# Performance work log

Hardware: AMD Instinct MI355X
Metric: run time of the kernel (lower is better)

Reference implementation:

```python
import jax, jax.numpy as jnp
import numpy as np

B, N, OBS, ACT, RET, E, OUT, K = 128, 1_000_000, 64, 16, 8, 64, 64, 16
MEM = OBS + ACT + RET  # 88


def setup_inputs() -> dict:
    key = jax.random.key(0)
    k0, k1, k2, k3 = jax.random.split(key, 4)
    obs = jax.random.normal(k0, (B, OBS), dtype=jnp.float32)
    memories = jax.random.normal(k1, (N, MEM), dtype=jnp.float32)
    W_obs = jax.random.normal(k2, (OBS, E), dtype=jnp.float32) * 0.05
    b_obs = jnp.zeros((E,), dtype=jnp.float32)
    W_out = jax.random.normal(k3, (E + ACT, OUT), dtype=jnp.float32) * 0.05
    b_out = jnp.zeros((OUT,), dtype=jnp.float32)
    return {"obs": obs, "memories": memories, "W_obs": W_obs, "b_obs": b_obs,
            "W_out": W_out, "b_out": b_out}


def reference(obs, memories, W_obs, b_obs, W_out, b_out):
    obs_len = W_obs.shape[0]          # 64
    embed_dim = W_obs.shape[1]        # 64
    act_len = W_out.shape[0] - embed_dim  # 16
    k = K

    obs_mem = memories[:, :obs_len]                              # [N, OBS]
    # f.normalize: L2-normalize each memory's observation part (eps as in torch)
    norm = jnp.maximum(jnp.linalg.norm(obs_mem, axis=-1, keepdims=True), 1e-12)
    m = obs_mem / norm                                           # [N, OBS], unit rows
    # squared L2 distance via expansion: |o|^2 + |m|^2 - 2 o.m  (|m|^2 == 1)
    # sqrt is monotonic, so top-k on squared distances gives identical indices.
    sq = (jnp.sum(obs * obs, axis=-1, keepdims=True) + 1.0
          - 2.0 * obs @ m.T)                                     # [B, N]
    _, idx = jax.lax.top_k(-sq, k)                               # k nearest, [B, k]

    sim_mems = memories[idx]                                     # [B, k, MEM]
    sim_act = sim_mems[..., obs_len:obs_len + act_len]           # [B, k, ACT]
    sim_ret = sim_mems[..., obs_len + act_len:]                  # [B, k, RET]
    ret_sum = jnp.sum(sim_ret, axis=-1)                          # [B, k]
    best = jnp.argmax(ret_sum, axis=-1)                          # [B]
    best_acts = jnp.take_along_axis(sim_act, best[:, None, None], axis=1)[:, 0]  # [B, ACT]

    obs_embeded = jnp.tanh(obs @ W_obs + b_obs)                  # [B, E]
    embed_best = jnp.concatenate([obs_embeded, best_acts], axis=-1)  # [B, E+ACT]
    logits = jnp.tanh(embed_best @ W_out + b_out)                # [B, OUT]
    return logits
```

## Files before the change

kernel.cpp:

```cpp
#include <hip/hip_runtime.h>
#include <cstdint>

#define B_    128
#define N_    1000000
#define OBS_  64
#define MEM_  88
#define ACT_  16
#define RET_  8
#define E_    64
#define OUT_  64
#define K_    16
#define CAP_  6144
#define P_    32
#define PCAP_ 256
#define CHUNKS_ (N_ / 16)
#define NBLK_  768
#define NWAVE_ (NBLK_ * 4)

typedef float    f32x4 __attribute__((ext_vector_type(4)));
typedef _Float16 f16x8 __attribute__((ext_vector_type(8)));
typedef uint32_t u32x4v __attribute__((ext_vector_type(4)));

__device__ __forceinline__ f16x8 pack8(float4 a, float4 b) {
    u32x4v u;
    u.x = __builtin_bit_cast(uint32_t, __builtin_amdgcn_cvt_pkrtz(a.x, a.y));
    u.y = __builtin_bit_cast(uint32_t, __builtin_amdgcn_cvt_pkrtz(a.z, a.w));
    u.z = __builtin_bit_cast(uint32_t, __builtin_amdgcn_cvt_pkrtz(b.x, b.y));
    u.w = __builtin_bit_cast(uint32_t, __builtin_amdgcn_cvt_pkrtz(b.z, b.w));
    return __builtin_bit_cast(f16x8, u);
}

__global__ __launch_bounds__(256, 3) void filter_kernel(const float* __restrict__ obs,
                                                        const float* __restrict__ memories,
                                                        int* __restrict__ cnt2,
                                                        int* __restrict__ cand2) {
    __shared__ float sThr[B_];

    const int tid  = threadIdx.x;
    const int lane = tid & 63;
    const int wv   = tid >> 6;
    const int fr   = lane & 15;
    const int fc   = lane >> 4;

    if (tid < B_) {
        const float4* orow = reinterpret_cast<const float4*>(obs + tid * OBS_);
        float s = 0.f;
        #pragma unroll
        for (int i = 0; i < 16; ++i) {
            float4 q = orow[i];
            s += q.x * q.x + q.y * q.y + q.z * q.z + q.w * q.w;
        }
        sThr[tid] = 0.45f * sqrtf(s);
    }

    f16x8 A0[8], A1[8];
    #pragma unroll
    for (int blk = 0; blk < 8; ++blk) {
        const float* p = obs + (blk * 16 + fr) * OBS_ + fc * 8;
        float4 q0 = *(const float4*)(p);
        float4 q1 = *(const float4*)(p + 4);
        float4 q2 = *(const float4*)(p + 32);
        float4 q3 = *(const float4*)(p + 36);
        A0[blk] = pack8(q0, q1);
        A1[blk] = pack8(q2, q3);
    }
    __syncthreads();

    float tmin[8];
    #pragma unroll
    for (int blk = 0; blk < 8; ++blk) {
        const float4 t = *reinterpret_cast<const float4*>(&sThr[blk * 16 + fc * 4]);
        tmin[blk] = fminf(fminf(t.x, t.y), fminf(t.z, t.w));
    }

    const int wid  = blockIdx.x * 4 + wv;
    const int part = wid & (P_ - 1);
    int* __restrict__ pcnt  = cnt2 + part * B_;
    int* __restrict__ pcand = cand2 + part * B_ * PCAP_;

    const int start = (int)((long long)wid * CHUNKS_ / NWAVE_);
    const int end   = (int)((long long)(wid + 1) * CHUNKS_ / NWAVE_);

    const int loff = fc * 8;

    float4 c0, c1, c2, c3, d0, d1, d2, d3;
    {
        const float* m = memories + (size_t)(start * 16 + fr) * MEM_ + loff;
        c0 = *(const float4*)(m);      c1 = *(const float4*)(m + 4);
        c2 = *(const float4*)(m + 32); c3 = *(const float4*)(m + 36);
    }
    {
        const float* m = memories + (size_t)((start + 1) * 16 + fr) * MEM_ + loff;
        d0 = *(const float4*)(m);      d1 = *(const float4*)(m + 4);
        d2 = *(const float4*)(m + 32); d3 = *(const float4*)(m + 36);
    }
    float nm;
    {
        float nq = c0.x*c0.x + c0.y*c0.y + c0.z*c0.z + c0.w*c0.w
                 + c1.x*c1.x + c1.y*c1.y + c1.z*c1.z + c1.w*c1.w
                 + c2.x*c2.x + c2.y*c2.y + c2.z*c2.z + c2.w*c2.w
                 + c3.x*c3.x + c3.y*c3.y + c3.z*c3.z + c3.w*c3.w;
        nq += __shfl_xor(nq, 16, 64);
        nq += __shfl_xor(nq, 32, 64);
        nm = sqrtf(nq);
    }

    for (int chunk = start; chunk < end; ++chunk) {
        int nc = chunk + 2;
        nc = (nc < end) ? nc : chunk;
        float4 e0, e1, e2, e3;
        {
            const float* m = memories + (size_t)(nc * 16 + fr) * MEM_ + loff;
            e0 = *(const float4*)(m);      e1 = *(const float4*)(m + 4);
            e2 = *(const float4*)(m + 32); e3 = *(const float4*)(m + 36);
        }

        float nqd = d0.x*d0.x + d0.y*d0.y + d0.z*d0.z + d0.w*d0.w
                  + d1.x*d1.x + d1.y*d1.y + d1.z*d1.z + d1.w*d1.w
                  + d2.x*d2.x + d2.y*d2.y + d2.z*d2.z + d2.w*d2.w
                  + d3.x*d3.x + d3.y*d3.y + d3.z*d3.z + d3.w*d3.w;
        nqd += __shfl_xor(nqd, 16, 64);
        nqd += __shfl_xor(nqd, 32, 64);

        const int gm = chunk * 16 + fr;
        const f16x8 b0 = pack8(c0, c1);
        const f16x8 b1 = pack8(c2, c3);

        #pragma unroll
        for (int blk = 0; blk < 8; ++blk) {
            f32x4 acc = {0.f, 0.f, 0.f, 0.f};
            acc = __builtin_amdgcn_mfma_f32_16x16x32_f16(A0[blk], b0, acc, 0, 0, 0);
            acc = __builtin_amdgcn_mfma_f32_16x16x32_f16(A1[blk], b1, acc, 0, 0, 0);
            const float m4 = fmaxf(fmaxf(acc[0], acc[1]), fmaxf(acc[2], acc[3]));
            if (m4 >= tmin[blk] * nm) {
                const float4 t = *reinterpret_cast<const float4*>(&sThr[blk * 16 + fc * 4]);
                const int rb = blk * 16 + fc * 4;
                if (acc[0] >= t.x * nm) { int p = atomicAdd(&pcnt[rb + 0], 1); if (p < PCAP_) pcand[(rb + 0) * PCAP_ + p] = gm; }
                if (acc[1] >= t.y * nm) { int p = atomicAdd(&pcnt[rb + 1], 1); if (p < PCAP_) pcand[(rb + 1) * PCAP_ + p] = gm; }
                if (acc[2] >= t.z * nm) { int p = atomicAdd(&pcnt[rb + 2], 1); if (p < PCAP_) pcand[(rb + 2) * PCAP_ + p] = gm; }
                if (acc[3] >= t.w * nm) { int p = atomicAdd(&pcnt[rb + 3], 1); if (p < PCAP_) pcand[(rb + 3) * PCAP_ + p] = gm; }
            }
        }

        c0 = d0; c1 = d1; c2 = d2; c3 = d3;
        d0 = e0; d1 = e1; d2 = e2; d3 = e3;
        nm = sqrtf(nqd);
    }
}

__global__ __launch_bounds__(256) void refine_kernel(const float* __restrict__ obs,
                                                     const float* __restrict__ memories,
                                                     const float* __restrict__ W_obs,
                                                     const float* __restrict__ b_obs,
                                                     const float* __restrict__ W_out,
                                                     const float* __restrict__ b_out,
                                                     const int* __restrict__ cnt2,
                                                     const int* __restrict__ cand2,
                                                     float* __restrict__ out) {
    __shared__ __align__(16) float sObs[OBS_];
    __shared__ unsigned long long sKey[CAP_];
    __shared__ int   pCnt[P_];
    __shared__ int   pBase[P_];
    __shared__ int   sN;
    __shared__ int   selIdx[K_];
    __shared__ float sRet[K_];
    __shared__ float sEmb[E_ + ACT_];
    __shared__ int   sBest;

    const int b   = blockIdx.x;
    const int tid = threadIdx.x;

    if (tid < OBS_) sObs[tid] = obs[b * OBS_ + tid];
    if (tid < P_) {
        int c = cnt2[tid * B_ + b];
        pCnt[tid] = (c > PCAP_) ? PCAP_ : c;
    }
    __syncthreads();
    if (tid == 0) {
        int off = 0;
        for (int p = 0; p < P_; ++p) { pBase[p] = off; off += pCnt[p]; }
        sN = (off > CAP_) ? CAP_ : off;
    }
    __syncthreads();
    const int n = sN;

    for (int p = 0; p < P_; ++p) {
        const int c = pCnt[p], base = pBase[p];
        for (int i = tid; i < c; i += 256) {
            int dst = base + i;
            if (dst < CAP_) sKey[dst] = (unsigned long long)(unsigned)cand2[(p * B_ + b) * PCAP_ + i];
        }
    }
    __syncthreads();

    for (int i = tid; i < n; i += 256) {
        int idx = (int)(unsigned)sKey[i];
        const float* mrow = memories + (size_t)idx * MEM_;
        float dot = 0.f, nq = 0.f;
        #pragma unroll
        for (int c = 0; c < OBS_; c += 4) {
            float4 mv = *reinterpret_cast<const float4*>(mrow + c);
            float4 ov = *reinterpret_cast<const float4*>(&sObs[c]);
            dot += mv.x * ov.x + mv.y * ov.y + mv.z * ov.z + mv.w * ov.w;
            nq  += mv.x * mv.x + mv.y * mv.y + mv.z * mv.z + mv.w * mv.w;
        }
        float sc = dot / fmaxf(sqrtf(nq), 1e-12f);
        uint32_t sb = __float_as_uint(sc);
        sb ^= (sb & 0x80000000u) ? 0xFFFFFFFFu : 0x80000000u;
        sKey[i] = ((unsigned long long)sb << 32) | (unsigned long long)(0xFFFFFFFFu - (uint32_t)idx);
    }
    __syncthreads();

    if (tid < 64) {
        for (int k = 0; k < K_; ++k) {
            unsigned long long best = 0ull; int bpos = -1;
            for (int i = tid; i < n; i += 64) {
                unsigned long long v = sKey[i];
                if (v > best) { best = v; bpos = i; }
            }
            #pragma unroll
            for (int off = 32; off > 0; off >>= 1) {
                unsigned long long ov = __shfl_xor(best, off, 64);
                int op = __shfl_xor(bpos, off, 64);
                if (ov > best) { best = ov; bpos = op; }
            }
            if (tid == 0) {
                selIdx[k] = (bpos >= 0) ? (int)(0xFFFFFFFFu - (uint32_t)(best & 0xFFFFFFFFull)) : -1;
                if (bpos >= 0) sKey[bpos] = 0ull;
            }
            __builtin_amdgcn_wave_barrier();
        }
    }
    __syncthreads();

    if (tid < K_) {
        int ix = selIdx[tid];
        float rs = -1e30f;
        if (ix >= 0) {
            rs = 0.f;
            #pragma unroll
            for (int j = 0; j < RET_; ++j)
                rs += memories[(size_t)ix * MEM_ + OBS_ + ACT_ + j];
        }
        sRet[tid] = rs;
    }
    __syncthreads();
    if (tid == 0) {
        float best = sRet[0]; int bk = 0;
        for (int k = 1; k < K_; ++k)
            if (sRet[k] > best) { best = sRet[k]; bk = k; }
        int bix = selIdx[bk];
        sBest = (bix >= 0) ? bix : 0;
    }
    __syncthreads();

    if (tid < E_) {
        float a = b_obs[tid];
        for (int c = 0; c < OBS_; ++c) a += sObs[c] * W_obs[c * E_ + tid];
        sEmb[tid] = tanhf(a);
    } else if (tid < E_ + ACT_) {
        int j = tid - E_;
        sEmb[tid] = memories[(size_t)sBest * MEM_ + OBS_ + j];
    }
    __syncthreads();

    if (tid < OUT_) {
        float a = b_out[tid];
        for (int c = 0; c < E_ + ACT_; ++c) a += sEmb[c] * W_out[c * OUT_ + tid];
        out[b * OUT_ + tid] = tanhf(a);
    }
}

extern "C" void kernel_launch(void* const* d_in, const int* in_sizes, int n_in,
                              void* d_out, int out_size, void* d_ws, size_t ws_size,
                              hipStream_t stream) {
    const float* obs      = (const float*)d_in[0];
    const float* memories = (const float*)d_in[1];
    const float* W_obs    = (const float*)d_in[2];
    const float* b_obs    = (const float*)d_in[3];
    const float* W_out    = (const float*)d_in[4];
    const float* b_out    = (const float*)d_in[5];
    float* out = (float*)d_out;

    char* ws    = (char*)d_ws;
    int*   cnt2 = (int*)ws;
    int*   cand2 = (int*)(ws + P_ * B_ * 4);

    hipMemsetAsync(cnt2, 0, P_ * B_ * sizeof(int), stream);
    filter_kernel<<<NBLK_, 256, 0, stream>>>(obs, memories, cnt2, cand2);
    refine_kernel<<<B_, 256, 0, stream>>>(obs, memories, W_obs, b_obs, W_out, b_out,
                                          cnt2, cand2, out);
}
```

Measured before the change: 111.6 us.

## Stage 32-row memory chunks through per-wave LDS with coalesced loads

```diff
diff --git a/kernel.cpp b/kernel.cpp
--- a/kernel.cpp
+++ b/kernel.cpp
@@ -13,13 +13,18 @@
 #define CAP_  6144
 #define P_    32
 #define PCAP_ 256
-#define CHUNKS_ (N_ / 16)
+#define ROWS_PC_ 32
+#define CHUNKS32_ (N_ / ROWS_PC_)
 #define NBLK_  768
 #define NWAVE_ (NBLK_ * 4)
+#define LDSROW_ 92
+#define LDSCHUNK_ (ROWS_PC_ * LDSROW_)
 
 typedef float    f32x4 __attribute__((ext_vector_type(4)));
 typedef _Float16 f16x8 __attribute__((ext_vector_type(8)));
 typedef uint32_t u32x4v __attribute__((ext_vector_type(4)));
+
+typedef struct { uint4 v[11]; } chunkregs;
 
 __device__ __forceinline__ f16x8 pack8(float4 a, float4 b) {
     u32x4v u;
@@ -35,6 +40,7 @@
                                                         int* __restrict__ cnt2,
                                                         int* __restrict__ cand2) {
     __shared__ float sThr[B_];
+    __shared__ __align__(16) float sMem[4 * LDSCHUNK_];
 
     const int tid  = threadIdx.x;
     const int lane = tid & 63;
@@ -78,73 +84,77 @@
     int* __restrict__ pcnt  = cnt2 + part * B_;
     int* __restrict__ pcand = cand2 + part * B_ * PCAP_;
 
-    const int start = (int)((long long)wid * CHUNKS_ / NWAVE_);
-    const int end   = (int)((long long)(wid + 1) * CHUNKS_ / NWAVE_);
-
-    const int loff = fc * 8;
-
-    float4 c0, c1, c2, c3, d0, d1, d2, d3;
+    const int start = (int)((long long)wid * CHUNKS32_ / NWAVE_);
+    const int end   = (int)((long long)(wid + 1) * CHUNKS32_ / NWAVE_);
+
+    float* __restrict__ lds = sMem + wv * LDSCHUNK_;
+    const uint4* __restrict__ mem4 = reinterpret_cast<const uint4*>(memories);
+
+    chunkregs G;
+
     {
-        const float* m = memories + (size_t)(start * 16 + fr) * MEM_ + loff;
-        c0 = *(const float4*)(m);      c1 = *(const float4*)(m + 4);
-        c2 = *(const float4*)(m + 32); c3 = *(const float4*)(m + 36);
-    }
-    {
-        const float* m = memories + (size_t)((start + 1) * 16 + fr) * MEM_ + loff;
-        d0 = *(const float4*)(m);      d1 = *(const float4*)(m + 4);
-        d2 = *(const float4*)(m + 32); d3 = *(const float4*)(m + 36);
-    }
-    float nm;
-    {
-        float nq = c0.x*c0.x + c0.y*c0.y + c0.z*c0.z + c0.w*c0.w
-                 + c1.x*c1.x + c1.y*c1.y + c1.z*c1.z + c1.w*c1.w
-                 + c2.x*c2.x + c2.y*c2.y + c2.z*c2.z + c2.w*c2.w
-                 + c3.x*c3.x + c3.y*c3.y + c3.z*c3.z + c3.w*c3.w;
-        nq += __shfl_xor(nq, 16, 64);
-        nq += __shfl_xor(nq, 32, 64);
-        nm = sqrtf(nq);
-    }
-
-    for (int chunk = start; chunk < end; ++chunk) {
-        int nc = chunk + 2;
-        nc = (nc < end) ? nc : chunk;
-        float4 e0, e1, e2, e3;
+        const uint4* src = mem4 + (size_t)start * 704;
+        #pragma unroll
+        for (int i = 0; i < 11; ++i) G.v[i] = src[i * 64 + lane];
+        #pragma unroll
+        for (int i = 0; i < 11; ++i) {
+            int j = i * 64 + lane;
+            int row = j / 22, slot = j - row * 22;
+            *reinterpret_cast<uint4*>(&lds[row * LDSROW_ + slot * 4]) = G.v[i];
+        }
+    }
+
+    for (int t = start; t < end; ++t) {
+        const int nt = (t + 1 < end) ? (t + 1) : t;
         {
-            const float* m = memories + (size_t)(nc * 16 + fr) * MEM_ + loff;
-            e0 = *(const float4*)(m);      e1 = *(const float4*)(m + 4);
-            e2 = *(const float4*)(m + 32); e3 = *(const float4*)(m + 36);
-        }
-
-        float nqd = d0.x*d0.x + d0.y*d0.y + d0.z*d0.z + d0.w*d0.w
-                  + d1.x*d1.x + d1.y*d1.y + d1.z*d1.z + d1.w*d1.w
-                  + d2.x*d2.x + d2.y*d2.y + d2.z*d2.z + d2.w*d2.w
-                  + d3.x*d3.x + d3.y*d3.y + d3.z*d3.z + d3.w*d3.w;
-        nqd += __shfl_xor(nqd, 16, 64);
-        nqd += __shfl_xor(nqd, 32, 64);
-
-        const int gm = chunk * 16 + fr;
-        const f16x8 b0 = pack8(c0, c1);
-        const f16x8 b1 = pack8(c2, c3);
-
-        #pragma unroll
-        for (int blk = 0; blk < 8; ++blk) {
-            f32x4 acc = {0.f, 0.f, 0.f, 0.f};
-            acc = __builtin_amdgcn_mfma_f32_16x16x32_f16(A0[blk], b0, acc, 0, 0, 0);
-            acc = __builtin_amdgcn_mfma_f32_16x16x32_f16(A1[blk], b1, acc, 0, 0, 0);
-            const float m4 = fmaxf(fmaxf(acc[0], acc[1]), fmaxf(acc[2], acc[3]));
-            if (m4 >= tmin[blk] * nm) {
-                const float4 t = *reinterpret_cast<const float4*>(&sThr[blk * 16 + fc * 4]);
-                const int rb = blk * 16 + fc * 4;
-                if (acc[0] >= t.x * nm) { int p = atomicAdd(&pcnt[rb + 0], 1); if (p < PCAP_) pcand[(rb + 0) * PCAP_ + p] = gm; }
-                if (acc[1] >= t.y * nm) { int p = atomicAdd(&pcnt[rb + 1], 1); if (p < PCAP_) pcand[(rb + 1) * PCAP_ + p] = gm; }
-                if (acc[2] >= t.z * nm) { int p = atomicAdd(&pcnt[rb + 2], 1); if (p < PCAP_) pcand[(rb + 2) * PCAP_ + p] = gm; }
-                if (acc[3] >= t.w * nm) { int p = atomicAdd(&pcnt[rb + 3], 1); if (p < PCAP_) pcand[(rb + 3) * PCAP_ + p] = gm; }
+            const uint4* src = mem4 + (size_t)nt * 704;
+            #pragma unroll
+            for (int i = 0; i < 11; ++i) G.v[i] = src[i * 64 + lane];
+        }
+
+        #pragma unroll
+        for (int g = 0; g < 2; ++g) {
+            const float* rbase = lds + (g * 16 + fr) * LDSROW_;
+            const float4 c0 = *reinterpret_cast<const float4*>(rbase + fc * 8);
+            const float4 c1 = *reinterpret_cast<const float4*>(rbase + fc * 8 + 4);
+            const float4 c2 = *reinterpret_cast<const float4*>(rbase + 32 + fc * 8);
+            const float4 c3 = *reinterpret_cast<const float4*>(rbase + 36 + fc * 8);
+
+            float nq = c0.x*c0.x + c0.y*c0.y + c0.z*c0.z + c0.w*c0.w
+                     + c1.x*c1.x + c1.y*c1.y + c1.z*c1.z + c1.w*c1.w
+                     + c2.x*c2.x + c2.y*c2.y + c2.z*c2.z + c2.w*c2.w
+                     + c3.x*c3.x + c3.y*c3.y + c3.z*c3.z + c3.w*c3.w;
+            nq += __shfl_xor(nq, 16, 64);
+            nq += __shfl_xor(nq, 32, 64);
+            const float nm = sqrtf(nq);
+            const int gm = t * ROWS_PC_ + g * 16 + fr;
+
+            const f16x8 b0 = pack8(c0, c1);
+            const f16x8 b1 = pack8(c2, c3);
+
+            #pragma unroll
+            for (int blk = 0; blk < 8; ++blk) {
+                f32x4 acc = {0.f, 0.f, 0.f, 0.f};
+                acc = __builtin_amdgcn_mfma_f32_16x16x32_f16(A0[blk], b0, acc, 0, 0, 0);
+                acc = __builtin_amdgcn_mfma_f32_16x16x32_f16(A1[blk], b1, acc, 0, 0, 0);
+                const float m4 = fmaxf(fmaxf(acc[0], acc[1]), fmaxf(acc[2], acc[3]));
+                if (m4 >= tmin[blk] * nm) {
+                    const float4 tq = *reinterpret_cast<const float4*>(&sThr[blk * 16 + fc * 4]);
+                    const int rb = blk * 16 + fc * 4;
+                    if (acc[0] >= tq.x * nm) { int p = atomicAdd(&pcnt[rb + 0], 1); if (p < PCAP_) pcand[(rb + 0) * PCAP_ + p] = gm; }
+                    if (acc[1] >= tq.y * nm) { int p = atomicAdd(&pcnt[rb + 1], 1); if (p < PCAP_) pcand[(rb + 1) * PCAP_ + p] = gm; }
+                    if (acc[2] >= tq.z * nm) { int p = atomicAdd(&pcnt[rb + 2], 1); if (p < PCAP_) pcand[(rb + 2) * PCAP_ + p] = gm; }
+                    if (acc[3] >= tq.w * nm) { int p = atomicAdd(&pcnt[rb + 3], 1); if (p < PCAP_) pcand[(rb + 3) * PCAP_ + p] = gm; }
+                }
             }
         }
 
-        c0 = d0; c1 = d1; c2 = d2; c3 = d3;
-        d0 = e0; d1 = e1; d2 = e2; d3 = e3;
-        nm = sqrtf(nqd);
+        #pragma unroll
+        for (int i = 0; i < 11; ++i) {
+            int j = i * 64 + lane;
+            int row = j / 22, slot = j - row * 22;
+            *reinterpret_cast<uint4*>(&lds[row * LDSROW_ + slot * 4]) = G.v[i];
+        }
     }
 }
 
```

New measurement: 262.3 us. +135.0%, slower.

## Buffer filter candidates in per-wave LDS and flush to global at end

Applied to the files above, without the earlier changes.

```diff
diff --git a/kernel.cpp b/kernel.cpp
--- a/kernel.cpp
+++ b/kernel.cpp
@@ -16,6 +16,7 @@
 #define CHUNKS_ (N_ / 16)
 #define NBLK_  768
 #define NWAVE_ (NBLK_ * 4)
+#define WCAP_  128
 
 typedef float    f32x4 __attribute__((ext_vector_type(4)));
 typedef _Float16 f16x8 __attribute__((ext_vector_type(8)));
@@ -35,6 +36,8 @@
                                                         int* __restrict__ cnt2,
                                                         int* __restrict__ cand2) {
     __shared__ float sThr[B_];
+    __shared__ int sCand[4][WCAP_];
+    __shared__ int sCnt[4];
 
     const int tid  = threadIdx.x;
     const int lane = tid & 63;
@@ -52,6 +55,7 @@
         }
         sThr[tid] = 0.45f * sqrtf(s);
     }
+    if (lane == 0) sCnt[wv] = 0;
 
     f16x8 A0[8], A1[8];
     #pragma unroll
@@ -73,24 +77,21 @@
         tmin[blk] = fminf(fminf(t.x, t.y), fminf(t.z, t.w));
     }
 
-    const int wid  = blockIdx.x * 4 + wv;
-    const int part = wid & (P_ - 1);
-    int* __restrict__ pcnt  = cnt2 + part * B_;
-    int* __restrict__ pcand = cand2 + part * B_ * PCAP_;
-
-    const int start = (int)((long long)wid * CHUNKS_ / NWAVE_);
-    const int end   = (int)((long long)(wid + 1) * CHUNKS_ / NWAVE_);
+    const int wid = blockIdx.x * 4 + wv;
+    int* __restrict__ myCand = &sCand[wv][0];
+    int* __restrict__ myCnt  = &sCnt[wv];
 
     const int loff = fc * 8;
 
     float4 c0, c1, c2, c3, d0, d1, d2, d3;
     {
-        const float* m = memories + (size_t)(start * 16 + fr) * MEM_ + loff;
+        const float* m = memories + (size_t)(wid * 16 + fr) * MEM_ + loff;
         c0 = *(const float4*)(m);      c1 = *(const float4*)(m + 4);
         c2 = *(const float4*)(m + 32); c3 = *(const float4*)(m + 36);
     }
     {
-        const float* m = memories + (size_t)((start + 1) * 16 + fr) * MEM_ + loff;
+        const int pc = (wid + NWAVE_ < CHUNKS_) ? (wid + NWAVE_) : wid;
+        const float* m = memories + (size_t)(pc * 16 + fr) * MEM_ + loff;
         d0 = *(const float4*)(m);      d1 = *(const float4*)(m + 4);
         d2 = *(const float4*)(m + 32); d3 = *(const float4*)(m + 36);
     }
@@ -105,9 +106,9 @@
         nm = sqrtf(nq);
     }
 
-    for (int chunk = start; chunk < end; ++chunk) {
-        int nc = chunk + 2;
-        nc = (nc < end) ? nc : chunk;
+    for (int chunk = wid; chunk < CHUNKS_; chunk += NWAVE_) {
+        int nc = chunk + 2 * NWAVE_;
+        nc = (nc < CHUNKS_) ? nc : chunk;
         float4 e0, e1, e2, e3;
         {
             const float* m = memories + (size_t)(nc * 16 + fr) * MEM_ + loff;
@@ -135,16 +136,34 @@
             if (m4 >= tmin[blk] * nm) {
                 const float4 t = *reinterpret_cast<const float4*>(&sThr[blk * 16 + fc * 4]);
                 const int rb = blk * 16 + fc * 4;
-                if (acc[0] >= t.x * nm) { int p = atomicAdd(&pcnt[rb + 0], 1); if (p < PCAP_) pcand[(rb + 0) * PCAP_ + p] = gm; }
-                if (acc[1] >= t.y * nm) { int p = atomicAdd(&pcnt[rb + 1], 1); if (p < PCAP_) pcand[(rb + 1) * PCAP_ + p] = gm; }
-                if (acc[2] >= t.z * nm) { int p = atomicAdd(&pcnt[rb + 2], 1); if (p < PCAP_) pcand[(rb + 2) * PCAP_ + p] = gm; }
-                if (acc[3] >= t.w * nm) { int p = atomicAdd(&pcnt[rb + 3], 1); if (p < PCAP_) pcand[(rb + 3) * PCAP_ + p] = gm; }
+                #pragma unroll
+                for (int j = 0; j < 4; ++j) {
+                    const float th = (j==0)?t.x:(j==1)?t.y:(j==2)?t.z:t.w;
+                    if (acc[j] >= th * nm) {
+                        int q = atomicAdd(myCnt, 1);
+                        if (q < WCAP_) myCand[q] = ((rb + j) << 20) | gm;
+                    }
+                }
             }
         }
 
         c0 = d0; c1 = d1; c2 = d2; c3 = d3;
         d0 = e0; d1 = e1; d2 = e2; d3 = e3;
         nm = sqrtf(nqd);
+    }
+
+    {
+        const int part = wid & (P_ - 1);
+        int* __restrict__ pcnt  = cnt2 + part * B_;
+        int* __restrict__ pcand = cand2 + part * B_ * PCAP_;
+        int n = *myCnt; if (n > WCAP_) n = WCAP_;
+        for (int i = lane; i < n; i += 64) {
+            const int e   = myCand[i];
+            const int row = e >> 20;
+            const int gm  = e & 0xFFFFF;
+            int q = atomicAdd(&pcnt[row], 1);
+            if (q < PCAP_) pcand[row * PCAP_ + q] = gm;
+        }
     }
 }
 
```

After: 105.0 us. 5.9% less time.
